# Optimization experiments

Measured on AMD Instinct MI355X. Metric: run time of the kernel, lower is better.

Reference implementation:

```python
import jax, jax.numpy as jnp
import numpy as np
import math

N = 5000; K = 30; E = N * K
C_S, C_Z, C_A = 256, 128, 16
H, DH, P, L = 4, 64, 8, 4
NUM_AA = 21
NUM_RBF = 16; D_MIN, D_MAX = 2.0, 22.0
EPS = 1e-8

def _ln(x):
    mu = jnp.mean(x, -1, keepdims=True)
    var = jnp.mean((x - mu) ** 2, -1, keepdims=True)
    return (x - mu) * jax.lax.rsqrt(var + 1e-5)

def _inv_apply(rot, trans, x):
    # rigid invert_apply: R^T (x - t); rot [n,3,3], trans [n,3], x [n,p,3]
    return jnp.einsum('nji,npj->npi', rot, x - trans[:, None, :])

def _rbf(d):
    mu = jnp.linspace(D_MIN, D_MAX, NUM_RBF)
    sigma = (D_MAX - D_MIN) / NUM_RBF
    return jnp.exp(-(((d[..., None] - mu) / sigma) ** 2))

def _dihedral_feats(bb):
    X = bb.reshape(-1, 3)  # [3N,3] N,CA,C chain
    dX = X[1:] - X[:-1]
    U = dX / (jnp.linalg.norm(dX, axis=-1, keepdims=True) + EPS)
    u2, u1, u0 = U[:-2], U[1:-1], U[2:]
    n2 = jnp.cross(u2, u1); n2 = n2 / (jnp.linalg.norm(n2, axis=-1, keepdims=True) + EPS)
    n1 = jnp.cross(u1, u0); n1 = n1 / (jnp.linalg.norm(n1, axis=-1, keepdims=True) + EPS)
    cosD = jnp.clip(jnp.sum(n2 * n1, -1), -1 + 1e-7, 1 - 1e-7)
    D = jnp.sign(jnp.sum(u2 * n1, -1)) * jnp.arccos(cosD)
    D = jnp.pad(D, (1, 2)).reshape(-1, 3)  # [N,3]
    return jnp.concatenate([jnp.cos(D), jnp.sin(D)], -1)  # [N,6]

def _virtual_cb(n, ca, c):
    b = ca - n; cc = c - ca; a = jnp.cross(b, cc)
    return -0.58273431 * a + 0.56802827 * b - 0.54067466 * cc + ca

def _prep(seq, atom14, rot, trans, res_mask, mgm_mask, noising_mask, atom14_exists, edge_index, atom_tab):
    res_f = res_mask.astype(jnp.float32)
    mgm_f = mgm_mask.astype(jnp.float32)
    bb = atom14[:, :3]
    dih = _dihedral_feats(bb)
    seq_oh = jax.nn.one_hot(seq, NUM_AA)
    node_vec = _inv_apply(rot, trans, atom14[:, :4])  # [N,4,3]
    node_raw = jnp.concatenate([dih, mgm_f[:, None], seq_oh * mgm_f[:, None], node_vec.reshape(N, -1)], -1) * res_f[:, None]
    sc = jnp.where(jnp.arange(14) >= 4, mgm_f[:, None], 1.0)  # zero hidden side-chain atoms
    am_f = jnp.where(jnp.arange(14) >= 4, mgm_mask[:, None], atom14_exists).astype(jnp.float32)
    atom_raw = atom_tab[seq] * sc[..., None]  # [N,14,9]
    dsti, srci = edge_index[0], edge_index[1]
    nsrc = noising_mask[srci].astype(jnp.float32); ndst = noising_mask[dsti].astype(jnp.float32)
    cb = _virtual_cb(bb[:, 0], bb[:, 1], bb[:, 2])
    bb4 = jnp.concatenate([bb, cb[:, None]], 1)  # [N,4,3]
    dist = jnp.linalg.norm(bb4[srci][:, :, None] - bb4[dsti][:, None, :] + EPS, axis=-1)  # [E,4,4]
    rbf = _rbf(dist).reshape(E, -1)  # [E,256]
    dpos = (dsti - srci).astype(jnp.float32)
    freq = jnp.exp(jnp.arange(0, 16, 2, dtype=jnp.float32) * (-math.log(10000.0) / 16))
    ang = dpos[:, None] * freq
    pe = jnp.concatenate([jnp.cos(ang), jnp.sin(ang)], -1)  # [E,16]
    bb_local = _inv_apply(rot, trans, bb4)
    src_local = bb_local[srci].reshape(E, -1) * (1 - nsrc)[:, None]
    dst_in_src = jnp.einsum('eji,epj->epi', rot[srci], bb4[dsti] - trans[srci][:, None, :]).reshape(E, -1) * (1 - ndst)[:, None]
    edge_mask = res_mask[srci] & res_mask[dsti]
    edge_raw = jnp.concatenate([ndst[:, None], nsrc[:, None], seq_oh[srci] * (1 - nsrc)[:, None], seq_oh[dsti] * (1 - ndst)[:, None], rbf, pe, src_local, dst_in_src], -1) * edge_mask.astype(jnp.float32)[:, None]
    return node_raw, edge_raw, atom_raw, res_f, am_f, edge_mask

def _mlp3(x, W1, W2, W3):
    return _ln(jax.nn.relu(jax.nn.relu(x @ W1) @ W2) @ W3)

def _net(node_raw, edge_raw, atom_raw, res_f, am_f, edge_mask, rot, trans, edge_index, Wn1, Wn2, Wn3, Wez1, Wez2, Wez3, Wa1, Wa2, Wa3, Wq, Wk, Wv, Wqp, Wkp, Wb, gamma, Wo, Wau, Wt1, Wt2, Wne, We1, We2, Wp1, Wp2, Wmu, Wlv):
    s = _mlp3(node_raw, Wn1, Wn2, Wn3)    # [N,256]
    z = _mlp3(edge_raw, Wez1, Wez2, Wez3) # [E,128]
    af = _mlp3(atom_raw, Wa1, Wa2, Wa3)   # [N,14,16]
    dsti, srci = edge_index[0], edge_index[1]
    em_f = edge_mask.astype(jnp.float32)
    w_pt = math.sqrt(2.0 / (9 * P)); w_l = math.sqrt(1.0 / 3.0)
    for l in range(L):
        q = (s @ Wq[l]).reshape(N, H, DH); k = (s @ Wk[l]).reshape(N, H, DH); v = (s @ Wv[l]).reshape(N, H, DH)
        qp = (s @ Wqp[l]).reshape(N, H, P, 3); kp = (s @ Wkp[l]).reshape(N, H, P, 3)
        qg = jnp.einsum('nij,nhpj->nhpi', rot, qp) + trans[:, None, None, :]
        kg = jnp.einsum('nij,nhpj->nhpi', rot, kp) + trans[:, None, None, :]
        logits = (jnp.sum(q[dsti] * k[srci], -1) * (w_l / math.sqrt(DH))
                  + w_l * (z @ Wb[l])
                  - 0.5 * w_pt * jax.nn.softplus(gamma[l]) * jnp.sum((qg[dsti] - kg[srci]) ** 2, (-2, -1)))
        logits = jnp.where(edge_mask[:, None], logits, -1e9)
        m = jax.ops.segment_max(logits, dsti, num_segments=N)
        a = jnp.exp(logits - m[dsti]) * em_f[:, None]
        a = a / (jax.ops.segment_sum(a, dsti, num_segments=N) + 1e-9)[dsti]
        ov = jax.ops.segment_sum(a[..., None] * v[srci], dsti, num_segments=N).reshape(N, -1)
        og = jax.ops.segment_sum(a[..., None, None] * kg[srci], dsti, num_segments=N)
        ol = jnp.einsum('nji,nhpj->nhpi', rot, og - trans[:, None, None, :])
        on = jnp.sqrt(jnp.sum(ol ** 2, -1) + EPS)
        s = _ln(s + jnp.concatenate([ov, ol.reshape(N, -1), on.reshape(N, -1)], -1) @ Wo[l])
        af = _ln(af + jnp.concatenate([af, jnp.broadcast_to(s[:, None, :], (N, 14, C_S))], -1) @ Wau[l])
        s = _ln(s + jax.nn.relu(s @ Wt1[l]) @ Wt2[l]) * res_f[:, None]
        h = s @ Wne[l]
        z = _ln(jax.nn.relu(jnp.concatenate([z, h[dsti], h[srci]], -1) @ We1[l]) @ We2[l]) * em_f[:, None]
        af = _ln(af + jax.nn.relu(af @ Wp1[l]) @ Wp2[l]) * am_f[..., None]
    return jnp.concatenate([s @ Wmu, s @ Wlv], -1)  # [N,512] = [mu | logvar]

def setup_inputs():
    ks = jax.random.split(jax.random.key(0), 40)
    w = lambda i, shp: jax.random.normal(ks[i], shp, dtype=jnp.float32) * 0.02
    return {
        'seq': jax.random.randint(ks[0], (N,), 0, NUM_AA, dtype=jnp.int32),
        'atom14': jax.random.normal(ks[1], (N, 14, 3), dtype=jnp.float32) * 3.0,
        'rot': jax.random.normal(ks[2], (N, 3, 3), dtype=jnp.float32),
        'trans': jax.random.normal(ks[3], (N, 3), dtype=jnp.float32) * 3.0,
        'res_mask': jnp.ones((N,), dtype=bool),
        'mgm_mask': jax.random.bernoulli(ks[4], 0.5, (N,)),
        'noising_mask': jax.random.bernoulli(ks[5], 0.5, (N,)),
        'atom14_exists': jnp.ones((N, 14), dtype=bool),
        'edge_index': jax.random.randint(ks[6], (2, E), 0, N, dtype=jnp.int32),
        'atom_tab': jax.random.uniform(ks[7], (NUM_AA + 1, 14, 9), dtype=jnp.float32),
        'Wn1': w(8, (40, 512)), 'Wn2': w(9, (512, 512)), 'Wn3': w(10, (512, 256)),
        'Wez1': w(11, (340, 256)), 'Wez2': w(12, (256, 256)), 'Wez3': w(13, (256, 128)),
        'Wa1': w(14, (9, 32)), 'Wa2': w(15, (32, 32)), 'Wa3': w(16, (32, 16)),
        'Wq': w(17, (L, 256, 256)), 'Wk': w(18, (L, 256, 256)), 'Wv': w(19, (L, 256, 256)),
        'Wqp': w(20, (L, 256, H * P * 3)), 'Wkp': w(21, (L, 256, H * P * 3)),
        'Wb': w(22, (L, 128, H)), 'gamma': w(23, (L, H)),
        'Wo': w(24, (L, H * (DH + 4 * P), 256)), 'Wau': w(25, (L, C_A + C_S, C_A)),
        'Wt1': w(26, (L, 256, 256)), 'Wt2': w(27, (L, 256, 256)),
        'Wne': w(28, (L, 256, 128)), 'We1': w(29, (L, 384, 256)), 'We2': w(30, (L, 256, 128)),
        'Wp1': w(31, (L, 16, 16)), 'Wp2': w(32, (L, 16, 16)),
        'Wmu': w(33, (256, 256)), 'Wlv': w(34, (256, 256)),
    }

def reference(seq, atom14, rot, trans, res_mask, mgm_mask, noising_mask, atom14_exists, edge_index, atom_tab, Wn1, Wn2, Wn3, Wez1, Wez2, Wez3, Wa1, Wa2, Wa3, Wq, Wk, Wv, Wqp, Wkp, Wb, gamma, Wo, Wau, Wt1, Wt2, Wne, We1, We2, Wp1, Wp2, Wmu, Wlv):
    prep = _prep(seq, atom14, rot, trans, res_mask, mgm_mask, noising_mask, atom14_exists, edge_index, atom_tab)
    return _net(*prep, rot, trans, edge_index, Wn1, Wn2, Wn3, Wez1, Wez2, Wez3, Wa1, Wa2, Wa3, Wq, Wk, Wv, Wqp, Wkp, Wb, gamma, Wo, Wau, Wt1, Wt2, Wne, We1, We2, Wp1, Wp2, Wmu, Wlv)
```

## Files before the change

kernel.cpp:

```cpp
#include <hip/hip_runtime.h>
#include <hip/hip_bf16.h>

#define NR 5000
#define EE 150000
#define NA14 (NR*14)
#define EPSF 1e-8f

typedef unsigned short ushort;
typedef __attribute__((ext_vector_type(8))) short bf16x8;
typedef __attribute__((ext_vector_type(4))) float f32x4;

#define GLDS16(gp, lp) __builtin_amdgcn_global_load_lds( \
    (__attribute__((address_space(1))) void*)(gp), \
    (__attribute__((address_space(3))) void*)(lp), 16, 0, 0)

static __device__ __forceinline__ float wsum64(float v) {
#pragma unroll
  for (int o = 1; o < 64; o <<= 1) v += __shfl_xor(v, o, 64);
  return v;
}
static __device__ __forceinline__ ushort f2b(float f) {
  union { float f; unsigned u; } x; x.f = f;
  unsigned r = (x.u + 0x7FFF + ((x.u >> 16) & 1)) >> 16;
  return (ushort)r;
// ... 111 lines not shown
  }
  nrawb[(size_t)n*64 + c] = f2b(v);
}

__global__ void k_atomraw(const int* __restrict__ seq, const int* __restrict__ mgm,
                          const int* __restrict__ a14ex, const float* __restrict__ atab,
                          float* __restrict__ araw, float* __restrict__ amf) {
  int idx = blockIdx.x * 256 + threadIdx.x;
  if (idx >= NA14) return;
  int n = idx / 14, a = idx - n*14;
  float mg = mgm[n] ? 1.f : 0.f;
  float sc = (a >= 4) ? mg : 1.f;
  const float* src = atab + ((size_t)seq[n]*14 + a) * 9;
#pragma unroll
  for (int j = 0; j < 9; ++j) araw[(size_t)idx*9 + j] = src[j] * sc;
  amf[idx] = (a >= 4) ? mg : (a14ex[idx] ? 1.f : 0.f);
}

__global__ void k_edgeraw(const int* __restrict__ dsti, const int* __restrict__ srci,
                          const int* __restrict__ seq, const int* __restrict__ rmask,
                          const int* __restrict__ nmask, const float* __restrict__ bb4,
                          const float* __restrict__ bbl, const float* __restrict__ rot,
                          const float* __restrict__ trans, ushort* __restrict__ eraw,
                          float* __restrict__ emf, int e0, int cnt) {
  int ei = blockIdx.x * 4 + (threadIdx.x >> 6);
  if (ei >= cnt) return;
  int e = e0 + ei;
  int l = threadIdx.x & 63;
  int d = dsti[e], s = srci[e];
  float em = (rmask[d] && rmask[s]) ? 1.f : 0.f;
  if (l == 0) emf[e] = em;
  float ns = nmask[s] ? 1.f : 0.f;
  float nd = nmask[d] ? 1.f : 0.f;
  ushort* out = eraw + (size_t)ei * 352;

  float dist;
  {
    int p = (l >> 2) & 3, q = l & 3;
    const float* Ps = bb4 + (size_t)s*12 + p*3;
    const float* Pd = bb4 + (size_t)d*12 + q*3;
    float dx = Ps[0]-Pd[0]+EPSF, dy = Ps[1]-Pd[1]+EPSF, dz = Ps[2]-Pd[2]+EPSF;
    dist = sqrtf(dx*dx + dy*dy + dz*dz);
  }
  {
    int q = (l >> 4) & 3;
    float mu = 2.f + (20.f / 15.f) * (float)(l & 15);
#pragma unroll
    for (int p = 0; p < 4; ++p) {
      float dd = __shfl(dist, p*4 + q, 64);
      float tt = (dd - mu) * 0.8f;
      out[44 + p*64 + l] = f2b(expf(-tt * tt) * em);
    }
  }
  if (l < 44) {
    float v;
    if (l == 0) v = nd;
    else if (l == 1) v = ns;
    else if (l < 23) v = (seq[s] == l - 2) ? (1.f - ns) : 0.f;
    else v = (seq[d] == l - 23) ? (1.f - nd) : 0.f;
    out[l] = f2b(v * em);
  }
  if (l < 52) {
    int c = 300 + l;
    float v;
    if (c < 316) {
      int f = c - 300;
      int j = (f < 8) ? f : (f - 8);
      float freq = expf((float)(2*j) * (-9.210340371976184f / 16.f));
      float ang = (float)(d - s) * freq;
      v = (f < 8) ? cosf(ang) : sinf(ang);
    } else if (c < 328) {
      v = bbl[(size_t)s*12 + (c - 316)] * (1.f - ns);
    } else if (c < 340) {
      int u = c - 328; int p = u / 3, i = u - p*3;
      const float* R = rot + (size_t)s*9;
      const float* t = trans + (size_t)s*3;
      const float* Pd = bb4 + (size_t)d*12 + p*3;
      v = (R[0*3+i]*(Pd[0]-t[0]) + R[1*3+i]*(Pd[1]-t[1]) + R[2*3+i]*(Pd[2]-t[2])) * (1.f - nd);
    } else v = 0.f;
    out[c] = f2b(v * em);
  }
}


__global__ void k_zero_int(int* __restrict__ p, int n) {
  int i = blockIdx.x * 256 + threadIdx.x;
  if (i < n) p[i] = 0;
}
__global__ void k_count(const int* __restrict__ dsti, int* __restrict__ cnt) {
  int e = blockIdx.x * 256 + threadIdx.x;
  if (e < EE) atomicAdd(&cnt[dsti[e]], 1);
}
__global__ void k_scan(const int* __restrict__ cnt, int* __restrict__ offs) {
  __shared__ int part[257];
  int t = threadIdx.x;
  const int chunk = (NR + 255) / 256;
  int b = t * chunk;
  int e = min(b + chunk, NR);
  int s = 0;
  for (int i = b; i < e; ++i) s += cnt[i];
  part[t] = s;
  __syncthreads();
  if (t == 0) {
    int r = 0;
    for (int i = 0; i < 256; ++i) { int c = part[i]; part[i] = r; r += c; }
    part[256] = r;
  }
  __syncthreads();
  int r = part[t];
  for (int i = b; i < e; ++i) { offs[i] = r; r += cnt[i]; }
  if (t == 0) offs[NR] = part[256];
}
__global__ void k_place(const int* __restrict__ dsti, const int* __restrict__ offs,
                        int* __restrict__ cnt, int* __restrict__ eord) {
  int e = blockIdx.x * 256 + threadIdx.x;
  if (e < EE) {
    int d = dsti[e];
    int pos = offs[d] + atomicAdd(&cnt[d], 1);
    eord[pos] = e;
  }
}
__global__ void k_sortwave(const int* __restrict__ offs, int* __restrict__ eord) {
  int n = blockIdx.x;
  int l = threadIdx.x;
  int b = offs[n], e = offs[n+1];
  int deg = e - b;
  if (deg <= 1) return;
  if (deg <= 64) {
    int v = (l < deg) ? eord[b + l] : 0x7FFFFFFF;
#pragma unroll
    for (int k = 2; k <= 64; k <<= 1) {
#pragma unroll
      for (int j = k >> 1; j > 0; j >>= 1) {
        int o = __shfl_xor(v, j, 64);
        bool up = ((l & k) == 0);
        bool first = ((l & j) == 0);
        int mn = min(v, o), mx = max(v, o);
        v = (first == up) ? mn : mx;
      }
    }
    if (l < deg) eord[b + l] = v;
  } else if (l == 0) {
    for (int i = b + 1; i < e; ++i) {
      int key = eord[i]; int j = i - 1;
      while (j >= b && eord[j] > key) { eord[j+1] = eord[j]; --j; }
      eord[j+1] = key;
    }
  }
}

__global__ void k_wT(const float* __restrict__ W, ushort* __restrict__ WT,
                     int K, int N, int Kpad, long sstride, long dstride, int L,
                     int perm) {
  long idx = (long)blockIdx.x * 256 + threadIdx.x;
  long per = (long)N * Kpad;
  if (idx >= per * L) return;
  int l = (int)(idx / per); long r = idx - (long)l * per;
  int n = (int)(r / Kpad), k = (int)(r - (long)n * Kpad);
  int ks = perm ? ((k & ~63) | ((k & 3) * 16 + ((k >> 2) & 15))) : k;
  WT[(size_t)l * dstride + (size_t)n * Kpad + k] =
      (ks < K) ? f2b(W[(size_t)l * sstride + (size_t)ks * N + n]) : (ushort)0;
}

__global__ void k_zero_us(ushort* __restrict__ p, int per, long stride, int L) {
  long idx = (long)blockIdx.x * 256 + threadIdx.x;
  if (idx >= (long)per * L) return;
  int l = (int)(idx / per); int r = (int)(idx - (long)l * per);
  p[(size_t)l * stride + r] = 0;
}

__global__ void k_wbT(const float* __restrict__ Wb, float* __restrict__ WbT) {
  int idx = blockIdx.x * 256 + threadIdx.x;
  if (idx >= 2048) return;
  int l = idx >> 9; int r = idx & 511; int h = r >> 7; int dim = r & 127;
  WbT[idx] = Wb[(size_t)l * 512 + dim * 4 + h];
}
__global__ void k_coef(const float* __restrict__ gam, float* __restrict__ coef) {
  int i = threadIdx.x;
  if (i < 16) coef[i] = 0.5f * (1.f / 6.f) * log1pf(expf(gam[i]));
}

template<int RELU, int OUTBF, int EPADD, int PERMOUT>
__global__ __launch_bounds__(256) void k_mgemm(
    const ushort* __restrict__ A, const ushort* __restrict__ BT,
    float* __restrict__ Cf, ushort* __restrict__ Cb,
    int M, int Ncols, int Kd, int lda,
    const ushort* __restrict__ HD, const ushort* __restrict__ HS,
    const int* __restrict__ dsti, const int* __restrict__ srci) {
  __shared__ __align__(16) ushort As[2][128][4][8];
  __shared__ __align__(16) ushort Bs[2][128][4][8];
  const int tid = threadIdx.x;
  const int lane = tid & 63;
  const int w = tid >> 6;
  const int wm = (w >> 1) * 64;
  const int wn = (w & 1) * 64;
  const int bm = blockIdx.x * 128;
  const int bn = blockIdx.y * 128;
  const int rl0 = tid >> 2;
  const int sl  = tid & 3;
  const int rl1 = rl0 + 64;
  const int ks0 = (sl - rl0 - (rl0 >> 2)) & 3;
  const int ks1 = (sl - rl1 - (rl1 >> 2)) & 3;
  int ar0 = bm + rl0; if (ar0 >= M) ar0 = M - 1;
  int ar1 = bm + rl1; if (ar1 >= M) ar1 = M - 1;
  const ushort* gA0 = A + (size_t)ar0 * lda + ks0 * 8;
  const ushort* gA1 = A + (size_t)ar1 * lda + ks1 * 8;
  const ushort* gB0 = BT + (size_t)(bn + rl0) * Kd + ks0 * 8;
  const ushort* gB1 = BT + (size_t)(bn + rl1) * Kd + ks1 * 8;

  auto stage = [&](int buf, int k0) {
    GLDS16(gA0 + k0, &As[buf][rl0][sl][0]);
    GLDS16(gB0 + k0, &Bs[buf][rl0][sl][0]);
    GLDS16(gA1 + k0, &As[buf][rl1][sl][0]);
    GLDS16(gB1 + k0, &Bs[buf][rl1][sl][0]);
  };

  f32x4 zero4 = {0.f, 0.f, 0.f, 0.f};
  f32x4 acc[4][4];
#pragma unroll
  for (int i = 0; i < 4; ++i)
#pragma unroll
    for (int j = 0; j < 4; ++j) acc[i][j] = zero4;

  stage(0, 0);
  asm volatile("s_waitcnt vmcnt(0)" ::: "memory");
  __builtin_amdgcn_s_barrier();

  const int nt = Kd >> 5;
  for (int t = 0; t < nt; ++t) {
    int cur = t & 1;
    if (t + 1 < nt) stage(cur ^ 1, (t + 1) << 5);
    {
      const int ksr = lane >> 4, lr = lane & 15;
      bf16x8 af[4], bf[4];
#pragma unroll
      for (int i = 0; i < 4; ++i) {
        int row = wm + i*16 + lr;
        int sa = (ksr + row + (row >> 2)) & 3;
        af[i] = *reinterpret_cast<const bf16x8*>(&As[cur][row][sa][0]);
      }
#pragma unroll
      for (int j = 0; j < 4; ++j) {
        int col = wn + j*16 + lr;
        int sb = (ksr + col + (col >> 2)) & 3;
        bf[j] = *reinterpret_cast<const bf16x8*>(&Bs[cur][col][sb][0]);
      }
#pragma unroll
      for (int i = 0; i < 4; ++i)
#pragma unroll
        for (int j = 0; j < 4; ++j)
          acc[i][j] = __builtin_amdgcn_mfma_f32_16x16x32_bf16(af[i], bf[j], acc[i][j], 0, 0, 0);
    }
    asm volatile("s_waitcnt vmcnt(0) lgkmcnt(0)" ::: "memory");
    __builtin_amdgcn_s_barrier();
  }

  int lr = lane & 15, lg = lane >> 4;
  if (PERMOUT) {
    const int pc = bn + wn + lr * 4;
#pragma unroll
    for (int i = 0; i < 4; ++i) {
#pragma unroll
      for (int rg = 0; rg < 4; ++rg) {
        int m = bm + wm + i*16 + lg*4 + rg;
        if (m >= M) continue;
        float v0 = acc[i][0][rg], v1 = acc[i][1][rg];
        float v2 = acc[i][2][rg], v3 = acc[i][3][rg];
        if (EPADD) {
          int de = dsti[m], se = srci[m];
          uint2 hd = *reinterpret_cast<const uint2*>(HD + (size_t)de * Ncols + pc);
          uint2 hs = *reinterpret_cast<const uint2*>(HS + (size_t)se * Ncols + pc);
          v0 += blo(hd.x) + blo(hs.x);
          v1 += bhi(hd.x) + bhi(hs.x);
          v2 += blo(hd.y) + blo(hs.y);
          v3 += bhi(hd.y) + bhi(hs.y);
        }
        if (RELU) {
          v0 = fmaxf(v0, 0.f); v1 = fmaxf(v1, 0.f);
          v2 = fmaxf(v2, 0.f); v3 = fmaxf(v3, 0.f);
        }
        uint2 p;
        p.x = (unsigned)f2b(v0) | ((unsigned)f2b(v1) << 16);
        p.y = (unsigned)f2b(v2) | ((unsigned)f2b(v3) << 16);
        *reinterpret_cast<uint2*>(Cb + (size_t)m * Ncols + pc) = p;
      }
    }
  } else {
#pragma unroll
    for (int i = 0; i < 4; ++i) {
#pragma unroll
      for (int rg = 0; rg < 4; ++rg) {
        int m = bm + wm + i*16 + lg*4 + rg;
        if (m >= M) continue;
#pragma unroll
        for (int j = 0; j < 4; ++j) {
          int cc = bn + wn + j*16 + lr;
          float v = acc[i][j][rg];
          if (RELU) v = fmaxf(v, 0.f);
          if (OUTBF) Cb[(size_t)m * Ncols + cc] = f2b(v);
          else       Cf[(size_t)m * Ncols + cc] = v;
        }
      }
    }
  }
}

__global__ void k_gemm(const float* __restrict__ A, const float* __restrict__ B,
                       float* __restrict__ C, int M, int Ncols, int Kd,
                       int ldc, int coff, int relu) {
  __shared__ float As[16][68];
  __shared__ float Bs[16][64];
  const int tid = threadIdx.x;
  const int bm = blockIdx.x * 64;
  const int bn = blockIdx.y * 64;
  const int tm = tid >> 4;
  const int tn = tid & 15;
  const int arow = tid >> 2;
  const int akq = (tid & 3) << 2;
  const int brow = tid >> 4;
  const int bcol = (tid & 15) << 2;
  float acc[4][4] = {{0.f}};
  const int am = bm + arow;
  for (int k0 = 0; k0 < Kd; k0 += 16) {
    float av[4];
#pragma unroll
    for (int j = 0; j < 4; ++j) {
      int k = k0 + akq + j;
      av[j] = (am < M && k < Kd) ? A[(size_t)am * Kd + k] : 0.f;
    }
#pragma unroll
    for (int j = 0; j < 4; ++j) As[akq + j][arow] = av[j];
    int kb = k0 + brow;
    float bv[4];
    if (kb < Kd) {
#pragma unroll
      for (int j = 0; j < 4; ++j) {
        int c = bn + bcol + j;
        bv[j] = (c < Ncols) ? B[(size_t)kb * Ncols + c] : 0.f;
      }
    } else { bv[0]=bv[1]=bv[2]=bv[3]=0.f; }
    *reinterpret_cast<float4*>(&Bs[brow][bcol]) = make_float4(bv[0],bv[1],bv[2],bv[3]);
    __syncthreads();
#pragma unroll
    for (int kk = 0; kk < 16; ++kk) {
      float4 a4 = *reinterpret_cast<const float4*>(&As[kk][tm << 2]);
      float4 b4 = *reinterpret_cast<const float4*>(&Bs[kk][tn << 2]);
      float aa[4] = {a4.x, a4.y, a4.z, a4.w};
      float bb[4] = {b4.x, b4.y, b4.z, b4.w};
#pragma unroll
      for (int i = 0; i < 4; ++i)
#pragma unroll
        for (int j = 0; j < 4; ++j)
          acc[i][j] = fmaf(aa[i], bb[j], acc[i][j]);
    }
    __syncthreads();
  }
#pragma unroll
  for (int i = 0; i < 4; ++i) {
    int m = bm + (tm << 2) + i;
    if (m >= M) continue;
#pragma unroll
    for (int j = 0; j < 4; ++j) {
      int c = bn + (tn << 2) + j;
      if (c >= Ncols) continue;
      float v = acc[i][j];
      if (relu) v = fmaxf(v, 0.f);
      C[(size_t)m * ldc + coff + c] = v;
    }
  }
}

__global__ void k_small_gemm(const float* __restrict__ A, const float* __restrict__ B,
                             float* __restrict__ C, int M, int Ncols, int Kd, int relu) {
  __shared__ float Ws[1024];
  int t = threadIdx.x;
  int nw = Kd * Ncols;
  for (int i = t; i < nw; i += 256) Ws[i] = B[i];
  __syncthreads();
  int rpb = 256 / Ncols;
  int r = blockIdx.x * rpb + t / Ncols;
  int c = t - (t / Ncols) * Ncols;
  if (r >= M || t >= rpb * Ncols) return;
  const float* a = A + (size_t)r * Kd;
  float s = 0.f;
  for (int k = 0; k < Kd; ++k) s = fmaf(a[k], Ws[k * Ncols + c], s);
  if (relu) s = fmaxf(s, 0.f);
  C[(size_t)r * Ncols + c] = s;
}

__global__ void k_ln(float* __restrict__ dst, ushort* __restrict__ dstb,
                     const float* __restrict__ res, const float* __restrict__ x,
                     const float* __restrict__ rowscale, int M) {
  int r = blockIdx.x * 4 + (threadIdx.x >> 6);
  if (r >= M) return;
  int l = threadIdx.x & 63;
  size_t base = (size_t)r * 256 + l * 4;
  float4 v = *reinterpret_cast<const float4*>(x + base);
  if (res) {
    float4 rv = *reinterpret_cast<const float4*>(res + base);
    v.x += rv.x; v.y += rv.y; v.z += rv.z; v.w += rv.w;
  }
  float s = wsum64(v.x + v.y + v.z + v.w);
  float mu = s * (1.f / 256.f);
  float d0 = v.x-mu, d1 = v.y-mu, d2 = v.z-mu, d3 = v.w-mu;
  float s2 = wsum64(d0*d0 + d1*d1 + d2*d2 + d3*d3);
  float rs = rsqrtf(s2 * (1.f / 256.f) + 1e-5f);
  float sc = rowscale ? rowscale[r] : 1.f;
  float o0 = d0*rs*sc, o1 = d1*rs*sc, o2 = d2*rs*sc, o3 = d3*rs*sc;
  *reinterpret_cast<float4*>(dst + base) = make_float4(o0, o1, o2, o3);
  if (dstb) {
    uint2 p;
    p.x = (unsigned)f2b(o0) | ((unsigned)f2b(o1) << 16);
    p.y = (unsigned)f2b(o2) | ((unsigned)f2b(o3) << 16);
    *reinterpret_cast<uint2*>(dstb + base) = p;
  }
}

__global__ void k_lnz(ushort* __restrict__ z, const float* __restrict__ rowscale) {
  int r = blockIdx.x * 4 + (threadIdx.x >> 6);
  int l = threadIdx.x & 63;
  size_t base = (size_t)r * 128 + l * 2;
  unsigned zw = *reinterpret_cast<const unsigned*>(z + base);
  float v0 = blo(zw), v1 = bhi(zw);
  float s = wsum64(v0 + v1);
  float mu = s * (1.f / 128.f);
  float d0 = v0 - mu, d1 = v1 - mu;
  float s2 = wsum64(d0*d0 + d1*d1);
  float rs = rsqrtf(s2 * (1.f / 128.f) + 1e-5f);
  float sc = rowscale ? rowscale[r] : 1.f;
  unsigned w = (unsigned)f2b(d0*rs*sc) | ((unsigned)f2b(d1*rs*sc) << 16);
  *reinterpret_cast<unsigned*>(z + base) = w;
}

__global__ void k_ln16(float* __restrict__ af, int M) {
  int r = blockIdx.x * 256 + threadIdx.x;
  if (r >= M) return;
  float x[16]; float s = 0.f;
#pragma unroll
  for (int j = 0; j < 16; ++j) { x[j] = af[(size_t)r*16 + j]; s += x[j]; }
  float mu = s * (1.f/16.f);
  float v = 0.f;
#pragma unroll
  for (int j = 0; j < 16; ++j) { float d = x[j]-mu; v += d*d; }
  float rs = rsqrtf(v * (1.f/16.f) + 1e-5f);
#pragma unroll
  for (int j = 0; j < 16; ++j) af[(size_t)r*16 + j] = (x[j]-mu)*rs;
}


__global__ void k_qg(const float* __restrict__ rot, const float* __restrict__ trans,
                     const float* __restrict__ pp,
                     float* __restrict__ qg, float* __restrict__ kg) {
  int idx = blockIdx.x * 256 + threadIdx.x;
  if (idx >= NR * 64) return;
  int n = idx >> 6; int w = (idx >> 5) & 1; int hp = idx & 31;
  const float* src = pp + (size_t)n*256 + (w ? 96 : 0) + hp*3;
  float* dstp = (w ? kg : qg) + (size_t)n*96 + hp*3;
  const float* R = rot + (size_t)n*9;
  const float* t = trans + (size_t)n*3;
  float s0 = src[0], s1 = src[1], s2 = src[2];
#pragma unroll
  for (int i = 0; i < 3; ++i)
    dstp[i] = R[i*3+0]*s0 + R[i*3+1]*s1 + R[i*3+2]*s2 + t[i];
}

__global__ void k_logits(const int* __restrict__ dsti, const int* __restrict__ srci,
                         const float* __restrict__ emf, const ushort* __restrict__ qkv,
                         const ushort* __restrict__ z,
                         const float* __restrict__ qg, const float* __restrict__ kg,
                         const float* __restrict__ WbT, const float* __restrict__ coef,
                         float* __restrict__ logits) {
  int e = blockIdx.x * 4 + (threadIdx.x >> 6);
  int l = threadIdx.x & 63;
  int hh = l >> 4, t = l & 15;
  int d = dsti[e], s = srci[e];
  const float wl = 0.57735026918962576f;
  const float qk_scale = wl * 0.125f;
  uint2 qw = *reinterpret_cast<const uint2*>(qkv + (size_t)d*768 + hh*64 + t*4);
  uint2 kw = *reinterpret_cast<const uint2*>(qkv + (size_t)s*768 + 256 + hh*64 + t*4);
  float acc = qk_scale * (blo(qw.x)*blo(kw.x) + bhi(qw.x)*bhi(kw.x)
                        + blo(qw.y)*blo(kw.y) + bhi(qw.y)*bhi(kw.y));
  {
    uint4 zw = *reinterpret_cast<const uint4*>(z + (size_t)e*128 + t*8);
    const float* wb = WbT + hh*128 + t*8;
    float4 w0 = *reinterpret_cast<const float4*>(wb);
    float4 w1 = *reinterpret_cast<const float4*>(wb + 4);
    float zsum = blo(zw.x)*w0.x + bhi(zw.x)*w0.y + blo(zw.y)*w0.z + bhi(zw.y)*w0.w
               + blo(zw.z)*w1.x + bhi(zw.z)*w1.y + blo(zw.w)*w1.z + bhi(zw.w)*w1.w;
    acc += wl * zsum;
  }
  {
    float cf = coef[hh];
    int c = hh*24 + t;
    float dq = qg[(size_t)d*96 + c] - kg[(size_t)s*96 + c];
    acc -= cf * dq * dq;
    if (t < 8) {
      int c2 = c + 16;
      float dq2 = qg[(size_t)d*96 + c2] - kg[(size_t)s*96 + c2];
      acc -= cf * dq2 * dq2;
    }
  }
#pragma unroll
  for (int o = 1; o < 16; o <<= 1) acc += __shfl_xor(acc, o, 64);
  if (t == 0) {
    float em = emf[e];
    logits[(size_t)e*4 + hh] = (em > 0.f) ? acc : -1e9f;
  }
}

__global__ void k_attn(const int* __restrict__ offs, const int* __restrict__ eord,
                       const int* __restrict__ srci, const float* __restrict__ logits,
                       const float* __restrict__ emf, const ushort* __restrict__ qkv,
                       const float* __restrict__ kg, ushort* __restrict__ catb,
                       float* __restrict__ og) {
  int n = blockIdx.x; int l = threadIdx.x;
  int e0 = offs[n], e1 = offs[n+1];
  float m[4] = {-1e30f,-1e30f,-1e30f,-1e30f};
  for (int i = e0; i < e1; ++i) {
    int e = eord[i];
#pragma unroll
    for (int h = 0; h < 4; ++h) m[h] = fmaxf(m[h], logits[(size_t)e*4 + h]);
  }
  float den[4] = {0.f,0.f,0.f,0.f};
  float accv[4] = {0.f,0.f,0.f,0.f};
  float acg0 = 0.f, acg1 = 0.f;
  int hg0 = l / 24;
  int hg1 = (64 + l) / 24;
  for (int i = e0; i < e1; ++i) {
    int e = eord[i]; int s = srci[e];
    float em = emf[e];
    float a[4];
#pragma unroll
    for (int h = 0; h < 4; ++h) {
      a[h] = expf(logits[(size_t)e*4 + h] - m[h]) * em;
      den[h] += a[h];
    }
#pragma unroll
    for (int j = 0; j < 4; ++j)
      accv[j] = fmaf(a[j], b2f(qkv[(size_t)s*768 + 512 + j*64 + l]), accv[j]);
    acg0 = fmaf(a[hg0], kg[(size_t)s*96 + l], acg0);
    if (l < 32) acg1 = fmaf(a[hg1], kg[(size_t)s*96 + 64 + l], acg1);
  }
#pragma unroll
  for (int j = 0; j < 4; ++j)
    catb[(size_t)n*384 + j*64 + l] = f2b(accv[j] / (den[j] + 1e-9f));
  og[(size_t)n*96 + l] = acg0 / (den[hg0] + 1e-9f);
  if (l < 32) og[(size_t)n*96 + 64 + l] = acg1 / (den[hg1] + 1e-9f);
}

__global__ void k_olon(const float* __restrict__ rot, const float* __restrict__ trans,
                       const float* __restrict__ og, ushort* __restrict__ catb) {
  int idx = blockIdx.x * 256 + threadIdx.x;
  if (idx >= NR * 32) return;
  int n = idx >> 5, hp = idx & 31;
  const float* R = rot + (size_t)n*9;
  const float* t = trans + (size_t)n*3;
  const float* o = og + (size_t)n*96 + hp*3;
  float d0 = o[0]-t[0], d1 = o[1]-t[1], d2 = o[2]-t[2];
  float ol[3];
#pragma unroll
  for (int i = 0; i < 3; ++i)
    ol[i] = R[0*3+i]*d0 + R[1*3+i]*d1 + R[2*3+i]*d2;
  ushort* cp = catb + (size_t)n*384;
  cp[256 + hp*3 + 0] = f2b(ol[0]);
  cp[256 + hp*3 + 1] = f2b(ol[1]);
  cp[256 + hp*3 + 2] = f2b(ol[2]);
  cp[352 + hp] = f2b(sqrtf(ol[0]*ol[0] + ol[1]*ol[1] + ol[2]*ol[2] + EPSF));
}

__global__ void k_af_wau(float* __restrict__ af, const float* __restrict__ WauA,
                         const float* __restrict__ t1) {
  __shared__ float W[256];
  int t = threadIdx.x;
  W[t] = WauA[t];
  __syncthreads();
  int r = blockIdx.x * 256 + t;
  if (r >= NA14) return;
  int n = r / 14;
  float x[16], y[16];
#pragma unroll
  for (int j = 0; j < 16; ++j) x[j] = af[(size_t)r*16 + j];
#pragma unroll
  for (int j = 0; j < 16; ++j) y[j] = t1[(size_t)n*16 + j];
#pragma unroll
  for (int k = 0; k < 16; ++k) {
    float xv = x[k];
#pragma unroll
    for (int j = 0; j < 16; ++j) y[j] = fmaf(xv, W[k*16 + j], y[j]);
  }
  float v[16]; float s = 0.f;
#pragma unroll
  for (int j = 0; j < 16; ++j) { v[j] = x[j] + y[j]; s += v[j]; }
  float mu = s * (1.f/16.f);
  float var = 0.f;
#pragma unroll
  for (int j = 0; j < 16; ++j) { float d = v[j]-mu; var += d*d; }
  float rs = rsqrtf(var * (1.f/16.f) + 1e-5f);
#pragma unroll
  for (int j = 0; j < 16; ++j) af[(size_t)r*16 + j] = (v[j]-mu)*rs;
}

__global__ void k_af_p(float* __restrict__ af, const float* __restrict__ Wp1,
                       const float* __restrict__ Wp2, const float* __restrict__ amf) {
  __shared__ float W1[256], W2[256];
  int t = threadIdx.x;
  W1[t] = Wp1[t]; W2[t] = Wp2[t];
  __syncthreads();
  int r = blockIdx.x * 256 + t;
  if (r >= NA14) return;
  float x[16];
#pragma unroll
  for (int j = 0; j < 16; ++j) x[j] = af[(size_t)r*16 + j];
  float h1[16];
#pragma unroll
  for (int j = 0; j < 16; ++j) h1[j] = 0.f;
#pragma unroll
  for (int k = 0; k < 16; ++k) {
    float xv = x[k];
#pragma unroll
    for (int j = 0; j < 16; ++j) h1[j] = fmaf(xv, W1[k*16 + j], h1[j]);
  }
#pragma unroll
  for (int j = 0; j < 16; ++j) h1[j] = fmaxf(h1[j], 0.f);
  float h2[16];
#pragma unroll
  for (int j = 0; j < 16; ++j) h2[j] = 0.f;
#pragma unroll
  for (int k = 0; k < 16; ++k) {
    float xv = h1[k];
#pragma unroll
    for (int j = 0; j < 16; ++j) h2[j] = fmaf(xv, W2[k*16 + j], h2[j]);
  }
  float v[16]; float s = 0.f;
#pragma unroll
  for (int j = 0; j < 16; ++j) { v[j] = x[j] + h2[j]; s += v[j]; }
  float mu = s * (1.f/16.f);
  float var = 0.f;
#pragma unroll
  for (int j = 0; j < 16; ++j) { float d = v[j]-mu; var += d*d; }
  float rs = rsqrtf(var * (1.f/16.f) + 1e-5f);
  float am = amf[r];
#pragma unroll
  for (int j = 0; j < 16; ++j) af[(size_t)r*16 + j] = (v[j]-mu)*rs*am;
}

__global__ void k_sentinel(float* __restrict__ out, float val) {
  if (threadIdx.x == 0 && blockIdx.x == 0) out[0] = val;
}


extern "C" void kernel_launch(void* const* d_in, const int* in_sizes, int n_in,
                              void* d_out, int out_size, void* d_ws, size_t ws_size,
                              hipStream_t stream) {
  (void)in_sizes; (void)n_in; (void)out_size;
  const int*   seq    = (const int*)  d_in[0];
  const float* atom14 = (const float*)d_in[1];
  const float* rot    = (const float*)d_in[2];
  const float* trans  = (const float*)d_in[3];
  const int*   rmask  = (const int*)  d_in[4];
  const int*   mgm    = (const int*)  d_in[5];
  const int*   nmask  = (const int*)  d_in[6];
  const int*   a14ex  = (const int*)  d_in[7];
  const int*   eidx   = (const int*)  d_in[8];
  const int*   dsti   = eidx;
  const int*   srci   = eidx + EE;
  const float* atab   = (const float*)d_in[9];
  const float* Wn1 = (const float*)d_in[10];
  const float* Wn2 = (const float*)d_in[11];
  const float* Wn3 = (const float*)d_in[12];
  const float* Wez1 = (const float*)d_in[13];
  const float* Wez2 = (const float*)d_in[14];
  const float* Wez3 = (const float*)d_in[15];
  const float* Wa1 = (const float*)d_in[16];
  const float* Wa2 = (const float*)d_in[17];
  const float* Wa3 = (const float*)d_in[18];
  const float* Wq  = (const float*)d_in[19];
  const float* Wk  = (const float*)d_in[20];
  const float* Wv  = (const float*)d_in[21];
  const float* Wqp = (const float*)d_in[22];
  const float* Wkp = (const float*)d_in[23];
  const float* Wb  = (const float*)d_in[24];
  const float* gam = (const float*)d_in[25];
  const float* Wo  = (const float*)d_in[26];
  const float* Wau = (const float*)d_in[27];
  const float* Wt1 = (const float*)d_in[28];
  const float* Wt2 = (const float*)d_in[29];
  const float* Wne = (const float*)d_in[30];
  const float* We1 = (const float*)d_in[31];
  const float* We2 = (const float*)d_in[32];
  const float* Wp1 = (const float*)d_in[33];
  const float* Wp2 = (const float*)d_in[34];
  const float* Wmu = (const float*)d_in[35];
  const float* Wlv = (const float*)d_in[36];
  float* out = (float*)d_out;

  float* ws = (float*)d_ws;
  size_t WSF = ws_size / sizeof(float);
  size_t off = 0;
  auto alloc = [&](size_t n) { n = (n + 3) & ~(size_t)3; float* p = ws + off; off += n; return p; };

  ushort* Zb  = (ushort*)alloc((size_t)EE * 64);
  float* S    = alloc((size_t)NR * 256);
  ushort* SB  = (ushort*)alloc((size_t)NR * 128);
  float* AF   = alloc((size_t)NA14 * 16);
  float* AMF  = alloc(NA14);
  float* EMF  = alloc(EE);
  float* LOG  = alloc((size_t)EE * 4);
  float* RESF = alloc(NR);
  float* DP   = alloc(3 * NR);
  float* BB4  = alloc((size_t)NR * 12);
  float* BBL  = alloc((size_t)NR * 12);
  ushort* NRAWB = (ushort*)alloc((size_t)NR * 32);
  float* ARAW = alloc((size_t)NA14 * 9);
  ushort* WezT1 = (ushort*)alloc(45056);
  ushort* WezT2 = (ushort*)alloc(32768);
  ushort* WezT3 = (ushort*)alloc(16384);
  ushort* We1zT = (ushort*)alloc(65536);
  ushort* We1dT = (ushort*)alloc(65536);
  ushort* We1sT = (ushort*)alloc(65536);
  ushort* We2T  = (ushort*)alloc(65536);
  ushort* WqkvT = (ushort*)alloc(393216);
  ushort* WppT  = (ushort*)alloc(131072);
  ushort* WoT   = (ushort*)alloc(196608);
  ushort* Wt1T  = (ushort*)alloc(131072);
  ushort* Wt2T  = (ushort*)alloc(131072);
  ushort* WneT  = (ushort*)alloc(65536);
  ushort* WmuLvT= (ushort*)alloc(65536);
  ushort* Wn1T  = (ushort*)alloc(16384);
  ushort* Wn2T  = (ushort*)alloc(131072);
  ushort* Wn3T  = (ushort*)alloc(65536);
  float* WBT  = alloc(2048);
  float* COEF = alloc(16);
  ushort* QKVB= (ushort*)alloc((size_t)NR * 384);
  float* PP   = alloc((size_t)NR * 256);
  float* QG   = alloc((size_t)NR * 96);
  float* KG   = alloc((size_t)NR * 96);
  ushort* CATB= (ushort*)alloc((size_t)NR * 192);
  float* OGb  = alloc((size_t)NR * 96);
  float* NBUF = alloc((size_t)NR * 256);
  ushort* HbB = (ushort*)alloc((size_t)NR * 64);
  ushort* HDb = (ushort*)alloc((size_t)NR * 128);
  ushort* HSb = (ushort*)alloc((size_t)NR * 128);
  float* T1   = alloc((size_t)NR * 16);
  ushort* NB1b = (ushort*)alloc((size_t)NR * 256);
  ushort* NB2b = (ushort*)alloc((size_t)NR * 256);
  ushort* TRHb = (ushort*)alloc((size_t)NR * 128);
  float* AH1  = alloc((size_t)NA14 * 32);
  float* AH2  = alloc((size_t)NA14 * 32);
  int* CNT  = (int*)alloc(NR);
  int* OFFS = (int*)alloc(NR + 1);
  int* EORD = (int*)alloc(EE);
  size_t fixedF = off;

  if (fixedF + (size_t)432 * 1024 > WSF) {
    k_sentinel<<<1, 64, 0, stream>>>(out, 1.0e6f * (float)(ws_size >> 20));
    return;
  }
  float* EAR = ws + fixedF;
  size_t arenaF = WSF - fixedF;
  int CH_P = (int)((arenaF / 432 > (size_t)EE) ? (size_t)EE : arenaF / 432);
  int CH_L = (int)((arenaF / 128 > (size_t)EE) ? (size_t)EE : arenaF / 128);
  ushort* ERb = (ushort*)EAR;
  ushort* B1b = ERb + (size_t)CH_P * 352;
  ushort* B2b = B1b + (size_t)CH_P * 256;
  ushort* EARb = (ushort*)EAR;

  auto wT = [&](const float* W, ushort* WTp, int K, int N, int Kpad,
                long ss, long ds, int L, int perm) {
    long tot = (long)N * Kpad * L;
    k_wT<<<(int)((tot + 255) / 256), 256, 0, stream>>>(W, WTp, K, N, Kpad, ss, ds, L, perm);
  };

  wT(Wez1, WezT1, 340, 256, 352, 0, 0, 1, 0);
  wT(Wez2, WezT2, 256, 256, 256, 0, 0, 1, 1);
  wT(Wez3, WezT3, 256, 128, 256, 0, 0, 1, 1);
  wT(Wn1, Wn1T, 40, 512, 64, 0, 0, 1, 0);
  wT(Wn2, Wn2T, 512, 512, 512, 0, 0, 1, 1);
  wT(Wn3, Wn3T, 512, 256, 512, 0, 0, 1, 1);
  wT(We1,         We1zT, 128, 256, 128, 98304, 32768, 4, 0);
  wT(We1 + 32768, We1dT, 128, 256, 128, 98304, 32768, 4, 0);
  wT(We1 + 65536, We1sT, 128, 256, 128, 98304, 32768, 4, 0);
  wT(We2, We2T, 256, 128, 256, 32768, 32768, 4, 1);
  wT(Wo,  WoT,  384, 256, 384, 98304, 98304, 4, 0);
  wT(Wt1, Wt1T, 256, 256, 256, 65536, 65536, 4, 0);
  wT(Wt2, Wt2T, 256, 256, 256, 65536, 65536, 4, 1);
  wT(Wne, WneT, 256, 128, 256, 32768, 32768, 4, 0);
  wT(Wmu, WmuLvT, 256, 256, 256, 0, 0, 1, 0);
  wT(Wlv, WmuLvT + 65536, 256, 256, 256, 0, 0, 1, 0);
  wT(Wq,  WqkvT + 0,       256, 256, 256, 65536, 196608, 4, 0);
  wT(Wk,  WqkvT + 65536,   256, 256, 256, 65536, 196608, 4, 0);
  wT(Wv,  WqkvT + 131072,  256, 256, 256, 65536, 196608, 4, 0);
  wT(Wqp, WppT + 0,        256,  96, 256, 24576, 65536, 4, 0);
  wT(Wkp, WppT + 24576,    256,  96, 256, 24576, 65536, 4, 0);
  k_zero_us<<<(64*256*4 + 255)/256, 256, 0, stream>>>(WppT + 49152, 64*256, 65536, 4);
  k_wbT<<<8, 256, 0, stream>>>(Wb, WBT);
  k_coef<<<1, 64, 0, stream>>>(gam, COEF);

  k_masks<<<(NR + 255) / 256, 256, 0, stream>>>(rmask, RESF);
  k_dihedral<<<(3 * NR + 255) / 256, 256, 0, stream>>>(atom14, DP);
  k_bb4<<<(NR + 255) / 256, 256, 0, stream>>>(atom14, rot, trans, BB4, BBL);
  k_noderaw<<<NR, 64, 0, stream>>>(seq, atom14, rot, trans, DP, rmask, mgm, NRAWB);
  k_atomraw<<<(NA14 + 255) / 256, 256, 0, stream>>>(seq, mgm, a14ex, atab, ARAW, AMF);

  {
    dim3 g1((NR + 127) / 128, 4), g2((NR + 127) / 128, 4), g3((NR + 127) / 128, 2);
    k_mgemm<1,1,0,1><<<g1, 256, 0, stream>>>(NRAWB, Wn1T, nullptr, NB1b, NR, 512, 64, 64,
                                             nullptr, nullptr, nullptr, nullptr);
    k_mgemm<1,1,0,1><<<g2, 256, 0, stream>>>(NB1b, Wn2T, nullptr, NB2b, NR, 512, 512, 512,
                                             nullptr, nullptr, nullptr, nullptr);
    k_mgemm<0,0,0,0><<<g3, 256, 0, stream>>>(NB2b, Wn3T, NBUF, nullptr, NR, 256, 512, 512,
                                             nullptr, nullptr, nullptr, nullptr);
  }
  k_ln<<<(NR + 3) / 4, 256, 0, stream>>>(S, SB, nullptr, NBUF, nullptr, NR);

  k_small_gemm<<<(NA14 + 7) / 8, 256, 0, stream>>>(ARAW, Wa1, AH1, NA14, 32, 9, 1);
  k_small_gemm<<<(NA14 + 7) / 8, 256, 0, stream>>>(AH1, Wa2, AH2, NA14, 32, 32, 1);
  k_small_gemm<<<(NA14 + 15) / 16, 256, 0, stream>>>(AH2, Wa3, AF, NA14, 16, 32, 0);
  k_ln16<<<(NA14 + 255) / 256, 256, 0, stream>>>(AF, NA14);

  k_zero_int<<<(NR + 255) / 256, 256, 0, stream>>>(CNT, NR);
  k_count<<<(EE + 255) / 256, 256, 0, stream>>>(dsti, CNT);
  k_scan<<<1, 256, 0, stream>>>(CNT, OFFS);
  k_zero_int<<<(NR + 255) / 256, 256, 0, stream>>>(CNT, NR);
  k_place<<<(EE + 255) / 256, 256, 0, stream>>>(dsti, OFFS, CNT, EORD);
  k_sortwave<<<NR, 64, 0, stream>>>(OFFS, EORD);

  for (int e0 = 0; e0 < EE; e0 += CH_P) {
    int cnt = (EE - e0 < CH_P) ? (EE - e0) : CH_P;
    k_edgeraw<<<(cnt + 3) / 4, 256, 0, stream>>>(dsti, srci, seq, rmask, nmask,
                                                 BB4, BBL, rot, trans, ERb, EMF, e0, cnt);
    dim3 g1((cnt + 127) / 128, 2), g2((cnt + 127) / 128, 2), g3((cnt + 127) / 128, 1);
    k_mgemm<1,1,0,1><<<g1, 256, 0, stream>>>(ERb, WezT1, nullptr, B1b, cnt, 256, 352, 352,
                                             nullptr, nullptr, nullptr, nullptr);
    k_mgemm<1,1,0,1><<<g2, 256, 0, stream>>>(B1b, WezT2, nullptr, B2b, cnt, 256, 256, 256,
                                             nullptr, nullptr, nullptr, nullptr);
    k_mgemm<0,1,0,0><<<g3, 256, 0, stream>>>(B2b, WezT3, nullptr, Zb + (size_t)e0 * 128,
                                             cnt, 128, 256, 256,
                                             nullptr, nullptr, nullptr, nullptr);
  }
  k_lnz<<<EE / 4, 256, 0, stream>>>(Zb, nullptr);

  for (int l = 0; l < 4; ++l) {
    const ushort* WqkvT_l = WqkvT + (size_t)l * 196608;
    const ushort* WppT_l  = WppT  + (size_t)l * 65536;
    const ushort* WoT_l = WoT + (size_t)l * 98304;
    const float* Wau_l = Wau + (size_t)l * 4352;
    const ushort* Wt1T_l = Wt1T + (size_t)l * 65536;
    const ushort* Wt2T_l = Wt2T + (size_t)l * 65536;
    const ushort* WneT_l = WneT + (size_t)l * 32768;
    const ushort* We1zT_l = We1zT + (size_t)l * 32768;
    const ushort* We1dT_l = We1dT + (size_t)l * 32768;
    const ushort* We1sT_l = We1sT + (size_t)l * 32768;
    const ushort* We2T_l = We2T + (size_t)l * 32768;
    const float* Wp1_l = Wp1 + (size_t)l * 256;
    const float* Wp2_l = Wp2 + (size_t)l * 256;

    {
      dim3 gq((NR + 127) / 128, 6);
      k_mgemm<0,1,0,0><<<gq, 256, 0, stream>>>(SB, WqkvT_l, nullptr, QKVB, NR, 768, 256, 256,
                                               nullptr, nullptr, nullptr, nullptr);
      dim3 gp((NR + 127) / 128, 2);
      k_mgemm<0,0,0,0><<<gp, 256, 0, stream>>>(SB, WppT_l, PP, nullptr, NR, 256, 256, 256,
                                               nullptr, nullptr, nullptr, nullptr);
    }
    k_qg<<<(NR * 64 + 255) / 256, 256, 0, stream>>>(rot, trans, PP, QG, KG);
    k_logits<<<EE / 4, 256, 0, stream>>>(dsti, srci, EMF, QKVB, Zb, QG, KG,
                                         WBT + (size_t)l * 512, COEF + (size_t)l * 4, LOG);
    k_attn<<<NR, 64, 0, stream>>>(OFFS, EORD, srci, LOG, EMF, QKVB, KG, CATB, OGb);
    k_olon<<<(NR * 32 + 255) / 256, 256, 0, stream>>>(rot, trans, OGb, CATB);
    {
      dim3 g((NR + 127) / 128, 2);
      k_mgemm<0,0,0,0><<<g, 256, 0, stream>>>(CATB, WoT_l, NBUF, nullptr, NR, 256, 384, 384,
                                              nullptr, nullptr, nullptr, nullptr);
    }
    k_ln<<<(NR + 3) / 4, 256, 0, stream>>>(S, SB, S, NBUF, nullptr, NR);
    {
      dim3 g((NR + 63) / 64, 1);
      k_gemm<<<g, 256, 0, stream>>>(S, Wau_l + 256, T1, NR, 16, 256, 16, 0, 0);
    }
    k_af_wau<<<(NA14 + 255) / 256, 256, 0, stream>>>(AF, Wau_l, T1);
    {
      dim3 g((NR + 127) / 128, 2);
      k_mgemm<1,1,0,1><<<g, 256, 0, stream>>>(SB, Wt1T_l, nullptr, TRHb, NR, 256, 256, 256,
                                              nullptr, nullptr, nullptr, nullptr);
      k_mgemm<0,0,0,0><<<g, 256, 0, stream>>>(TRHb, Wt2T_l, NBUF, nullptr, NR, 256, 256, 256,
                                              nullptr, nullptr, nullptr, nullptr);
    }
    k_ln<<<(NR + 3) / 4, 256, 0, stream>>>(S, SB, S, NBUF, RESF, NR);
    {
      dim3 g((NR + 127) / 128, 1);
      k_mgemm<0,1,0,0><<<g, 256, 0, stream>>>(SB, WneT_l, nullptr, HbB, NR, 128, 256, 256,
                                              nullptr, nullptr, nullptr, nullptr);
    }
    {
      dim3 g((NR + 127) / 128, 2);
      k_mgemm<0,1,0,1><<<g, 256, 0, stream>>>(HbB, We1dT_l, nullptr, HDb, NR, 256, 128, 128,
                                              nullptr, nullptr, nullptr, nullptr);
      k_mgemm<0,1,0,1><<<g, 256, 0, stream>>>(HbB, We1sT_l, nullptr, HSb, NR, 256, 128, 128,
                                              nullptr, nullptr, nullptr, nullptr);
    }
    for (int e0 = 0; e0 < EE; e0 += CH_L) {
      int cnt = (EE - e0 < CH_L) ? (EE - e0) : CH_L;
      dim3 g1((cnt + 127) / 128, 2), g2((cnt + 127) / 128, 1);
      k_mgemm<1,1,1,1><<<g1, 256, 0, stream>>>(Zb + (size_t)e0 * 128, We1zT_l, nullptr, EARb,
                                               cnt, 256, 128, 128,
                                               HDb, HSb, dsti + e0, srci + e0);
      k_mgemm<0,1,0,0><<<g2, 256, 0, stream>>>(EARb, We2T_l, nullptr, Zb + (size_t)e0 * 128,
                                               cnt, 128, 256, 256,
                                               nullptr, nullptr, nullptr, nullptr);
    }
    k_lnz<<<EE / 4, 256, 0, stream>>>(Zb, EMF);
    k_af_p<<<(NA14 + 255) / 256, 256, 0, stream>>>(AF, Wp1_l, Wp2_l, AMF);
  }

  {
    dim3 g((NR + 127) / 128, 4);
    k_mgemm<0,0,0,0><<<g, 256, 0, stream>>>(SB, WmuLvT, out, nullptr, NR, 512, 256, 256,
                                            nullptr, nullptr, nullptr, nullptr);
  }
}
```

Baseline: 1.922 ms.

## Fuse edge MLP GEMMs, gather-add, ReLU and LayerNorm into one kernel

Replaces the per-layer edge update (two chunked GEMM launches plus a separate LayerNorm kernel) with one kernel per 128-edge tile. The kernel computes the first GEMM with the node-feature gather and ReLU, keeps the 256-wide hidden tile in swizzled LDS, runs the second GEMM, then applies LayerNorm and the edge mask in registers before writing Z back in place. This removes the global round trip of the 150k×256 hidden activation, the separate LN pass over Z, and extra launches. In exchange it uses 64KB of LDS per block, which limits occupancy, and it reads B weights straight from global memory inside the MFMA loop.

```diff
diff --git a/kernel.cpp b/kernel.cpp
--- a/kernel.cpp
+++ b/kernel.cpp
@@ -437,6 +437,136 @@
         }
       }
     }
+  }
+}
+
+__global__ __launch_bounds__(256) void k_zfused(
+    ushort* __restrict__ Zb, const ushort* __restrict__ W1zT,
+    const ushort* __restrict__ W2T,
+    const ushort* __restrict__ HD, const ushort* __restrict__ HS,
+    const int* __restrict__ dsti, const int* __restrict__ srci,
+    const float* __restrict__ emf, int M) {
+  __shared__ __align__(16) ushort EARl[128 * 256];
+  const int tid = threadIdx.x;
+  const int lane = tid & 63;
+  const int w = tid >> 6;
+  const int wm = w * 32;
+  const int bm = blockIdx.x * 128;
+  const int lr = lane & 15, lg = lane >> 4;
+
+  f32x4 zero4 = {0.f, 0.f, 0.f, 0.f};
+  f32x4 acc1[2][16];
+#pragma unroll
+  for (int i = 0; i < 2; ++i)
+#pragma unroll
+    for (int j = 0; j < 16; ++j) acc1[i][j] = zero4;
+
+  bf16x8 af[2][4];
+#pragma unroll
+  for (int i = 0; i < 2; ++i) {
+    int m = bm + wm + i*16 + lr; if (m >= M) m = M - 1;
+#pragma unroll
+    for (int kk = 0; kk < 4; ++kk)
+      af[i][kk] = *reinterpret_cast<const bf16x8*>(Zb + (size_t)m*128 + kk*32 + lg*8);
+  }
+#pragma unroll
+  for (int kk = 0; kk < 4; ++kk) {
+#pragma unroll
+    for (int j = 0; j < 16; ++j) {
+      bf16x8 bf = *reinterpret_cast<const bf16x8*>(W1zT + (size_t)(j*16+lr)*128 + kk*32 + lg*8);
+#pragma unroll
+      for (int i = 0; i < 2; ++i)
+        acc1[i][j] = __builtin_amdgcn_mfma_f32_16x16x32_bf16(af[i][kk], bf, acc1[i][j], 0, 0, 0);
+    }
+  }
+
+#pragma unroll
+  for (int i = 0; i < 2; ++i) {
+#pragma unroll
+    for (int rg = 0; rg < 4; ++rg) {
+      int row = wm + i*16 + lg*4 + rg;
+      int m = bm + row; if (m >= M) m = M - 1;
+      int de = dsti[m], se = srci[m];
+      int sx = (row & 7) << 1;
+#pragma unroll
+      for (int b = 0; b < 4; ++b) {
+        int pc = b*64 + lr*4;
+        float v0 = acc1[i][b*4+0][rg], v1 = acc1[i][b*4+1][rg];
+        float v2 = acc1[i][b*4+2][rg], v3 = acc1[i][b*4+3][rg];
+        uint2 hd = *reinterpret_cast<const uint2*>(HD + (size_t)de * 256 + pc);
+        uint2 hs = *reinterpret_cast<const uint2*>(HS + (size_t)se * 256 + pc);
+        v0 = fmaxf(v0 + blo(hd.x) + blo(hs.x), 0.f);
+        v1 = fmaxf(v1 + bhi(hd.x) + bhi(hs.x), 0.f);
+        v2 = fmaxf(v2 + blo(hd.y) + blo(hs.y), 0.f);
+        v3 = fmaxf(v3 + bhi(hd.y) + bhi(hs.y), 0.f);
+        uint2 p;
+        p.x = (unsigned)f2b(v0) | ((unsigned)f2b(v1) << 16);
+        p.y = (unsigned)f2b(v2) | ((unsigned)f2b(v3) << 16);
+        int gi = (b*16 + lr) ^ sx;
+        *reinterpret_cast<uint2*>(EARl + row*256 + gi*4) = p;
+      }
+    }
+  }
+  __syncthreads();
+
+  f32x4 acc2[2][8];
+#pragma unroll
+  for (int i = 0; i < 2; ++i)
+#pragma unroll
+    for (int j = 0; j < 8; ++j) acc2[i][j] = zero4;
+#pragma unroll
+  for (int kk = 0; kk < 8; ++kk) {
+    bf16x8 a2[2];
+#pragma unroll
+    for (int i = 0; i < 2; ++i) {
+      int row = wm + i*16 + lr;
+      int gi = (kk*8 + lg*2) ^ ((row & 7) << 1);
+      a2[i] = *reinterpret_cast<const bf16x8*>(EARl + row*256 + gi*4);
+    }
+#pragma unroll
+    for (int j = 0; j < 8; ++j) {
+      bf16x8 b2 = *reinterpret_cast<const bf16x8*>(W2T + (size_t)(j*16+lr)*256 + kk*32 + lg*8);
+#pragma unroll
+      for (int i = 0; i < 2; ++i)
+        acc2[i][j] = __builtin_amdgcn_mfma_f32_16x16x32_bf16(a2[i], b2, acc2[i][j], 0, 0, 0);
+    }
+  }
+  __syncthreads();
+
+  ushort* OUT = EARl;
+#pragma unroll
+  for (int i = 0; i < 2; ++i) {
+#pragma unroll
+    for (int rg = 0; rg < 4; ++rg) {
+      int row = wm + i*16 + lg*4 + rg;
+      int m = bm + row; int mc = (m >= M) ? (M - 1) : m;
+      float s = 0.f;
+#pragma unroll
+      for (int j = 0; j < 8; ++j) s += acc2[i][j][rg];
+#pragma unroll
+      for (int o = 1; o < 16; o <<= 1) s += __shfl_xor(s, o, 64);
+      float mu = s * (1.f / 128.f);
+      float vs = 0.f;
+#pragma unroll
+      for (int j = 0; j < 8; ++j) { float d = acc2[i][j][rg] - mu; vs += d*d; }
+#pragma unroll
+      for (int o = 1; o < 16; o <<= 1) vs += __shfl_xor(vs, o, 64);
+      float rs = rsqrtf(vs * (1.f / 128.f) + 1e-5f);
+      float sc = emf[mc];
+#pragma unroll
+      for (int j = 0; j < 8; ++j)
+        OUT[row*128 + j*16 + lr] = f2b((acc2[i][j][rg] - mu) * rs * sc);
+    }
+  }
+  __syncthreads();
+#pragma unroll
+  for (int u = 0; u < 8; ++u) {
+    int idx = tid + u * 256;
+    int row = idx >> 4; int co = (idx & 15) * 8;
+    int m = bm + row;
+    if (m < M)
+      *reinterpret_cast<uint4*>(Zb + (size_t)m*128 + co) =
+          *reinterpret_cast<const uint4*>(OUT + row*128 + co);
   }
 }
 
@@ -894,11 +1024,9 @@
   float* EAR = ws + fixedF;
   size_t arenaF = WSF - fixedF;
   int CH_P = (int)((arenaF / 432 > (size_t)EE) ? (size_t)EE : arenaF / 432);
-  int CH_L = (int)((arenaF / 128 > (size_t)EE) ? (size_t)EE : arenaF / 128);
   ushort* ERb = (ushort*)EAR;
   ushort* B1b = ERb + (size_t)CH_P * 352;
   ushort* B2b = B1b + (size_t)CH_P * 256;
-  ushort* EARb = (ushort*)EAR;
 
   auto wT = [&](const float* W, ushort* WTp, int K, int N, int Kpad,
                 long ss, long ds, int L, int perm) {
@@ -1034,17 +1162,8 @@
       k_mgemm<0,1,0,1><<<g, 256, 0, stream>>>(HbB, We1sT_l, nullptr, HSb, NR, 256, 128, 128,
                                               nullptr, nullptr, nullptr, nullptr);
     }
-    for (int e0 = 0; e0 < EE; e0 += CH_L) {
-      int cnt = (EE - e0 < CH_L) ? (EE - e0) : CH_L;
-      dim3 g1((cnt + 127) / 128, 2), g2((cnt + 127) / 128, 1);
-      k_mgemm<1,1,1,1><<<g1, 256, 0, stream>>>(Zb + (size_t)e0 * 128, We1zT_l, nullptr, EARb,
-                                               cnt, 256, 128, 128,
-                                               HDb, HSb, dsti + e0, srci + e0);
-      k_mgemm<0,1,0,0><<<g2, 256, 0, stream>>>(EARb, We2T_l, nullptr, Zb + (size_t)e0 * 128,
-                                               cnt, 128, 256, 256,
-                                               nullptr, nullptr, nullptr, nullptr);
-    }
-    k_lnz<<<EE / 4, 256, 0, stream>>>(Zb, EMF);
+    k_zfused<<<(EE + 127) / 128, 256, 0, stream>>>(Zb, We1zT_l, We2T_l, HDb, HSb,
+                                                   dsti, srci, EMF, EE);
     k_af_p<<<(NA14 + 255) / 256, 256, 0, stream>>>(AF, Wp1_l, Wp2_l, AMF);
   }
 
```

After: 2.329 ms. 1.21x slower.
